# Kernel tuning notes

Hardware: AMD Instinct MI355X
Metric: run time of the kernel (lower is better)

The kernel has to match this reference:

```python
import jax, jax.numpy as jnp
import numpy as np

DIM = 384
HEADS = 12
WIN = (7, 7)
N = WIN[0] * WIN[1]
B = 4096
NW = 64  # number of windows sharing one mask


def _relative_position_index(win):
    wh, ww = win
    coords = np.stack(np.meshgrid(np.arange(wh), np.arange(ww), indexing='ij'))  # (2,wh,ww)
    flat = coords.reshape(2, -1)                                                 # (2, N)
    rel = flat[:, :, None] - flat[:, None, :]                                    # (2, N, N)
    rel = rel.transpose(1, 2, 0).astype(np.int64)
    rel[:, :, 0] += wh - 1
    rel[:, :, 1] += ww - 1
    rel[:, :, 0] *= 2 * ww - 1
    return jnp.asarray(rel.sum(-1), dtype=jnp.int32)                             # (N, N)


def setup_inputs() -> dict:
    key = jax.random.key(0)
    ks = jax.random.split(key, 7)
    std = 0.02
    return {
        'x': jax.random.normal(ks[0], (B, N, DIM), jnp.float32),
        'mask': jax.random.normal(ks[1], (NW, N, N), jnp.float32),
        'qkv_w': jax.random.normal(ks[2], (3 * DIM, DIM), jnp.float32) * std,
        'qkv_b': jnp.zeros((3 * DIM,), jnp.float32),
        'bias_table': jax.random.normal(ks[3], ((2 * WIN[0] - 1) * (2 * WIN[1] - 1), HEADS), jnp.float32) * std,
        'proj_w': jax.random.normal(ks[4], (DIM, DIM), jnp.float32) * std,
        'proj_b': jnp.zeros((DIM,), jnp.float32),
        'rel_idx': _relative_position_index(WIN),
    }


def reference(x, mask, qkv_w, qkv_b, bias_table, proj_w, proj_b, rel_idx):
    B_, n, c = x.shape
    h = HEADS
    d = c // h
    scale = d ** -0.5

    qkv = x @ qkv_w.T + qkv_b                                  # (B_, N, 3C)
    qkv = qkv.reshape(B_, n, 3, h, d).transpose(2, 0, 3, 1, 4)  # (3, B_, H, N, D)
    q, k, v = qkv[0], qkv[1], qkv[2]

    attn = jnp.einsum('bhnd,bhmd->bhnm', q, k) * scale          # (B_, H, N, N)

    bias = bias_table[rel_idx]                                  # (N, N, H)
    attn = attn + bias.transpose(2, 0, 1)[None]                 # add (1, H, N, N)

    nW = mask.shape[0]
    attn = attn.reshape(B_ // nW, nW, h, n, n) + mask[None, :, None]
    attn = attn.reshape(B_, h, n, n)

    attn = jax.nn.softmax(attn, axis=-1)
    out = jnp.einsum('bhnm,bhmd->bhnd', attn, v)                # (B_, H, N, D)
    out = out.transpose(0, 2, 1, 3).reshape(B_, n, c)
    return out @ proj_w.T + proj_b
```

## Files before the change

kernel.cpp:

```cpp
#include <hip/hip_runtime.h>

typedef __bf16 bf16;
typedef __bf16 bf16x4 __attribute__((ext_vector_type(4)));
typedef __bf16 bf16x8 __attribute__((ext_vector_type(8)));
typedef float f32x4 __attribute__((ext_vector_type(4)));
typedef float f32x16 __attribute__((ext_vector_type(16)));
typedef int i32x2 __attribute__((ext_vector_type(2)));
typedef unsigned int u32;

#define DIMC 384
#define NHEADS 12
#define NTOK 49
#define NWINB 4096
#define MROWS (NWINB*NTOK)

#define MFMA32(A,B,C) __builtin_amdgcn_mfma_f32_32x32x16_bf16(A,B,C,0,0,0)

#define GLOAD16(gsrc, lbase) \
  __builtin_amdgcn_global_load_lds( \
      (const __attribute__((address_space(1))) u32*)(gsrc), \
      (__attribute__((address_space(3))) u32*)(lbase), 16, 0, 0)

__global__ __launch_bounds__(256) void k_convert(const float4* __restrict__ in,
                                                 bf16x4* __restrict__ out, int n4) {
  int stride = gridDim.x * blockDim.x;
  for (int i = blockIdx.x * blockDim.x + threadIdx.x; i < n4; i += stride) {
    float4 v = in[i];
    bf16x4 o;
    o[0] = (bf16)v.x; o[1] = (bf16)v.y; o[2] = (bf16)v.z; o[3] = (bf16)v.w;
    out[i] = o;
  }
}

__global__ __launch_bounds__(256) void k_biasT(const float* __restrict__ table,
                                               const int* __restrict__ rel,
                                               float* __restrict__ outp) {
  int i = blockIdx.x * 256 + threadIdx.x;
  if (i < NHEADS * NTOK * NTOK) {
    int h = i / (NTOK * NTOK), r2 = i - h * (NTOK * NTOK);
    int key = r2 / NTOK, q = r2 - key * NTOK;
    outp[i] = table[rel[q * NTOK + key] * NHEADS + h];
  }
}

__global__ __launch_bounds__(256) void k_maskT(const float* __restrict__ mask,
                                               float* __restrict__ outp) {
  int i = blockIdx.x * 256 + threadIdx.x;
  if (i < 64 * NTOK * NTOK) {
    int w = i / (NTOK * NTOK), r2 = i - w * (NTOK * NTOK);
    int key = r2 / NTOK, q = r2 - key * NTOK;
    outp[i] = mask[(w * NTOK + q) * NTOK + key];
  }
}

template <int MODE>
__global__ __launch_bounds__(256) void k_gemm(const bf16* __restrict__ A,
                                              const bf16* __restrict__ Bw,
                                              const float* __restrict__ bias,
                                              bf16* __restrict__ oQ, bf16* __restrict__ oK,
                                              bf16* __restrict__ oV, float* __restrict__ oP) {
  __shared__ __align__(16) bf16 lA[2][64 * 64];
  __shared__ __align__(16) bf16 lB[2][128 * 64];
  const int t = threadIdx.x;
  const int l = t & 63;
  const int wv = t >> 6;
  const int wr = wv >> 1, wc = wv & 1;

  const u32 NXB = MODE == 0 ? 9 : 3;
  const u32 nwg = NXB * (MROWS / 64);
  u32 lin = blockIdx.y * gridDim.x + blockIdx.x;
  u32 logical = (lin & 7) * (nwg >> 3) + (lin >> 3);
  const int n0 = (int)(logical % NXB) * 128;
  const int m0 = (int)(logical / NXB) * 64;

  const int lr = l & 15, lg = l >> 4;

  const int srowA = wv * 16 + (l >> 3);
  const int srowB = wv * 32 + (l >> 3);
  const int scolb = (l & 7) * 16;

  f32x4 acc[2][4] = {};

#define STAGE(BUF, K0)                                                            \
  {                                                                               \
    _Pragma("unroll") for (int i = 0; i < 2; ++i) {                               \
      int row = srowA + i * 8;                                                    \
      int sc = (scolb ^ ((row & 7) << 4)) >> 1;                                   \
      GLOAD16(&A[(size_t)(m0 + row) * DIMC + (K0) + sc],                          \
              &lA[BUF][wv * 1024 + i * 512]);                                     \
    }                                                                             \
    _Pragma("unroll") for (int i = 0; i < 4; ++i) {                               \
      int row = srowB + i * 8;                                                    \
      int sc = (scolb ^ ((row & 7) << 4)) >> 1;                                   \
      GLOAD16(&Bw[(size_t)(n0 + row) * DIMC + (K0) + sc],                         \
              &lB[BUF][wv * 2048 + i * 512]);                                     \
    }                                                                             \
  }

  STAGE(0, 0);

#pragma unroll
  for (int tt = 0; tt < 6; ++tt) {
    const int cur = tt & 1;
    if (tt > 0) __builtin_amdgcn_s_barrier();
    if (tt < 5) {
      STAGE(cur ^ 1, (tt + 1) * 64);
      asm volatile("s_waitcnt vmcnt(6)" ::: "memory");
    } else {
      asm volatile("s_waitcnt vmcnt(0)" ::: "memory");
    }
    __builtin_amdgcn_s_barrier();

#pragma unroll
    for (int kk = 0; kk < 64; kk += 32) {
      bf16x8 af[2], bfv[4];
#pragma unroll
      for (int f = 0; f < 2; ++f) {
        int row = wr * 32 + f * 16 + lr;
        int cb = (kk + lg * 8) * 2;
        af[f] = *reinterpret_cast<const bf16x8*>(
            &lA[cur][row * 64 + ((cb ^ ((row & 7) << 4)) >> 1)]);
      }
#pragma unroll
      for (int f = 0; f < 4; ++f) {
        int row = wc * 64 + f * 16 + lr;
        int cb = (kk + lg * 8) * 2;
        bfv[f] = *reinterpret_cast<const bf16x8*>(
            &lB[cur][row * 64 + ((cb ^ ((row & 7) << 4)) >> 1)]);
      }
#pragma unroll
      for (int fm = 0; fm < 2; ++fm)
#pragma unroll
        for (int fn = 0; fn < 4; ++fn)
          acc[fm][fn] = __builtin_amdgcn_mfma_f32_16x16x32_bf16(af[fm], bfv[fn], acc[fm][fn], 0, 0, 0);
    }
  }
#undef STAGE

  const int cbase = n0 + wc * 64;
  const bf16* dummy;
  bf16* dst;
  int col0;
  if (MODE == 0) {
    int which = cbase / 384;
    dst = which == 0 ? oQ : (which == 1 ? oK : oV);
    col0 = cbase - which * 384;
  }
#pragma unroll
  for (int fn = 0; fn < 4; ++fn) {
    int c = cbase + fn * 16 + lr;
    float bc = bias[c];
#pragma unroll
    for (int fm = 0; fm < 2; ++fm) {
#pragma unroll
      for (int r = 0; r < 4; ++r) {
        int m = m0 + wr * 32 + fm * 16 + lg * 4 + r;
        float v = acc[fm][fn][r] + bc;
        if (MODE == 0) {
          dst[(size_t)m * 384 + col0 + fn * 16 + lr] = (bf16)v;
        } else {
          oP[(size_t)m * 384 + c] = v;
        }
      }
    }
  }
  (void)dummy;
}

__global__ __launch_bounds__(256, 4) void k_attn(const bf16* __restrict__ Q,
                                                 const bf16* __restrict__ K,
                                                 const bf16* __restrict__ V,
                                                 const float* __restrict__ biasT,
                                                 const float* __restrict__ maskT,
                                                 bf16* __restrict__ H) {
  __shared__ __align__(16) bf16 Vl[4][32 * 72];
  const int t = threadIdx.x, l = t & 63, wv = t >> 6;
  const int p = blockIdx.x * 4 + wv;
  const int b = p / 12, h = p - b * 12;
  const int w = b & 63;
  const size_t rbase = (size_t)b * 49 * 384 + h * 32;
  const int c = l & 31, b5 = l >> 5;
  bf16* vl = Vl[wv];

  {
    bf16x4 z = {};
    for (int i = l; i < 128; i += 64) {
      int d = i >> 2, kq = 48 + (i & 3) * 4;
      *reinterpret_cast<bf16x4*>(&vl[d * 72 + kq]) = z;
    }
  }
  for (int i = l; i < 392; i += 64) {
    int key = i >> 3, dc = (i & 7) * 4;
    bf16x4 vv = *reinterpret_cast<const bf16x4*>(&V[rbase + (size_t)key * 384 + dc]);
#pragma unroll
    for (int j = 0; j < 4; ++j) vl[(dc + j) * 72 + key] = vv[j];
  }

  bf16x8 kf[2][2], qf[2][2];
#pragma unroll
  for (int f = 0; f < 2; ++f) {
    int row = f * 32 + c; if (row > 48) row = 48;
#pragma unroll
    for (int kd = 0; kd < 2; ++kd) {
      kf[f][kd] = *reinterpret_cast<const bf16x8*>(&K[rbase + (size_t)row * 384 + kd * 16 + b5 * 8]);
      qf[f][kd] = *reinterpret_cast<const bf16x8*>(&Q[rbase + (size_t)row * 384 + kd * 16 + b5 * 8]);
    }
  }

  const float scale = 0.17677669529663689f;
  const float* bT = biasT + h * 2401;
  const float* mT = maskT + w * 2401;

#pragma unroll
  for (int fn = 0; fn < 2; ++fn) {
    f32x16 s0 = {}, s1 = {};
    s0 = MFMA32(kf[0][0], qf[fn][0], s0);
    s0 = MFMA32(kf[0][1], qf[fn][1], s0);
    s1 = MFMA32(kf[1][0], qf[fn][0], s1);
    s1 = MFMA32(kf[1][1], qf[fn][1], s1);

    int q = fn * 32 + c;
    int qc = q > 48 ? 48 : q;

    float vals[32];
    float vmax = -1e30f;
#pragma unroll
    for (int fm = 0; fm < 2; ++fm) {
#pragma unroll
      for (int r = 0; r < 16; ++r) {
        int key = fm * 32 + (r & 3) + 8 * (r >> 2) + 4 * b5;
        float sv = fm ? s1[r] : s0[r];
        float v;
        if (key < 49) {
          float cm = bT[key * 49 + qc] + mT[key * 49 + qc];
          v = fmaf(sv, scale, cm);
        } else {
          v = -1e30f;
        }
        vals[fm * 16 + r] = v;
        vmax = fmaxf(vmax, v);
      }
    }
    vmax = fmaxf(vmax, __shfl_xor(vmax, 32));
    float sum = 0.f;
#pragma unroll
    for (int i = 0; i < 32; ++i) {
      float e = __expf(vals[i] - vmax);
      vals[i] = e;
      sum += e;
    }
    sum += __shfl_xor(sum, 32);
    float inv = 1.f / sum;

    f32x16 o = {};
#pragma unroll
    for (int kk = 0; kk < 4; ++kk) {
      int ib = (kk >> 1) * 16 + 8 * (kk & 1);
      union { bf16 hh[2]; u32 u; } cv;
      u32 A0, A1, B0, B1;
      cv.hh[0] = (bf16)(vals[ib + 0] * inv); cv.hh[1] = (bf16)(vals[ib + 1] * inv); A0 = cv.u;
      cv.hh[0] = (bf16)(vals[ib + 2] * inv); cv.hh[1] = (bf16)(vals[ib + 3] * inv); A1 = cv.u;
      cv.hh[0] = (bf16)(vals[ib + 4] * inv); cv.hh[1] = (bf16)(vals[ib + 5] * inv); B0 = cv.u;
      cv.hh[0] = (bf16)(vals[ib + 6] * inv); cv.hh[1] = (bf16)(vals[ib + 7] * inv); B1 = cv.u;
      i32x2 sw0 = __builtin_amdgcn_permlane32_swap((int)A0, (int)B0, false, false);
      i32x2 sw1 = __builtin_amdgcn_permlane32_swap((int)A1, (int)B1, false, false);
      union { u32 d[4]; bf16x8 v8; } pa;
      pa.d[0] = (u32)sw0[0]; pa.d[1] = (u32)sw1[0];
      pa.d[2] = (u32)sw0[1]; pa.d[3] = (u32)sw1[1];
      bf16x8 vf = *reinterpret_cast<const bf16x8*>(&vl[c * 72 + kk * 16 + b5 * 8]);
      o = MFMA32(pa.v8, vf, o);
    }

#pragma unroll
    for (int r = 0; r < 16; ++r) {
      int qrow = fn * 32 + (r & 3) + 8 * (r >> 2) + 4 * b5;
      if (qrow < 49)
        H[((size_t)b * 49 + qrow) * 384 + h * 32 + c] = (bf16)o[r];
    }
  }
}

extern "C" void kernel_launch(void* const* d_in, const int* in_sizes, int n_in,
                              void* d_out, int out_size, void* d_ws, size_t ws_size,
                              hipStream_t stream) {
  const float* x     = (const float*)d_in[0];
  const float* mask  = (const float*)d_in[1];
  const float* qkvw  = (const float*)d_in[2];
  const float* qkvb  = (const float*)d_in[3];
  const float* btab  = (const float*)d_in[4];
  const float* projw = (const float*)d_in[5];
  const float* projb = (const float*)d_in[6];
  const int*   rel   = (const int*)d_in[7];
  float* out = (float*)d_out;

  const size_t NELEM = (size_t)MROWS * DIMC;
  char* ws = (char*)d_ws;
  bf16*  xb    = (bf16*)ws;
  bf16*  vb    = (bf16*)(ws + 154140672);
  float* biasT = (float*)(ws + 308281344);
  bf16*  wqkv  = (bf16*)(ws + 308396800);
  float* maskT = (float*)(ws + 308396800);
  bf16*  wproj = (bf16*)(ws + 309281536);
  bf16* qb = (bf16*)d_out;
  bf16* kb = qb + NELEM;

  k_convert<<<2048, 256, 0, stream>>>((const float4*)x, (bf16x4*)xb, (int)(NELEM / 4));
  k_convert<<<432, 256, 0, stream>>>((const float4*)qkvw, (bf16x4*)wqkv, 3 * DIMC * DIMC / 4);
  k_convert<<<144, 256, 0, stream>>>((const float4*)projw, (bf16x4*)wproj, DIMC * DIMC / 4);
  k_biasT<<<(NHEADS * NTOK * NTOK + 255) / 256, 256, 0, stream>>>(btab, rel, biasT);

  k_gemm<0><<<dim3(9, MROWS / 64), 256, 0, stream>>>(xb, wqkv, qkvb, qb, kb, vb, nullptr);
  k_maskT<<<(64 * NTOK * NTOK + 255) / 256, 256, 0, stream>>>(mask, maskT);
  k_attn<<<(NWINB * NHEADS) / 4, 256, 0, stream>>>(qb, kb, vb, biasT, maskT, xb);
  k_gemm<1><<<dim3(3, MROWS / 64), 256, 0, stream>>>(xb, wproj, projb, nullptr, nullptr, nullptr, out);
}
```

Before: 889.9 us.

## Fuse window attention with output projection in one per-window kernel

Adds k_attn_proj, where each block handles one window: it computes all 12 heads' attention into a swizzled 64x384 bf16 LDS tile and then runs the output projection from LDS, writing the final fp32 output directly. This drops the global write and re-read of the attention output and the separate projection GEMM launch. Q and K now go to workspace instead of the output buffer, so the fused path only runs when the workspace is large enough, with the old path kept as a fallback. The cost is about 53KB of LDS per block, which lowers occupancy, and projection weights read straight from global or L2 with no LDS staging.

Measured after the change: 969.4 us. 1.09x slower.

```diff
diff --git a/kernel.cpp b/kernel.cpp
--- a/kernel.cpp
+++ b/kernel.cpp
@@ -138,9 +138,8 @@
 #undef STAGE
 
   const int cbase = n0 + wc * 64;
-  const bf16* dummy;
-  bf16* dst;
-  int col0;
+  bf16* dst = nullptr;
+  int col0 = 0;
   if (MODE == 0) {
     int which = cbase / 384;
     dst = which == 0 ? oQ : (which == 1 ? oK : oV);
@@ -164,7 +163,6 @@
       }
     }
   }
-  (void)dummy;
 }
 
 __global__ __launch_bounds__(256, 4) void k_attn(const bf16* __restrict__ Q,
@@ -280,6 +278,156 @@
   }
 }
 
+__global__ __launch_bounds__(256) void k_attn_proj(
+    const bf16* __restrict__ Q, const bf16* __restrict__ K,
+    const bf16* __restrict__ V, const float* __restrict__ biasT,
+    const float* __restrict__ maskT, const bf16* __restrict__ Wp,
+    const float* __restrict__ projb, float* __restrict__ OUT) {
+  __shared__ __align__(16) bf16 Vl[4][32 * 72];
+  __shared__ __align__(16) bf16 hl[64 * 384];
+  const int t = threadIdx.x, l = t & 63, wv = t >> 6;
+  const int b = blockIdx.x;
+  const int w = b & 63;
+  const int c = l & 31, b5 = l >> 5;
+  bf16* vl = Vl[wv];
+  const float scale = 0.17677669529663689f;
+  const float* mT = maskT + w * 2401;
+
+  {
+    bf16x4 z = {};
+    for (int i = l; i < 128; i += 64) {
+      int d = i >> 2, kq = 48 + (i & 3) * 4;
+      *reinterpret_cast<bf16x4*>(&vl[d * 72 + kq]) = z;
+    }
+  }
+
+  for (int hi = 0; hi < 3; ++hi) {
+    const int h = hi * 4 + wv;
+    const size_t rbase = (size_t)b * 49 * 384 + h * 32;
+    const float* bT = biasT + h * 2401;
+
+    for (int i = l; i < 392; i += 64) {
+      int key = i >> 3, dc = (i & 7) * 4;
+      bf16x4 vv = *reinterpret_cast<const bf16x4*>(&V[rbase + (size_t)key * 384 + dc]);
+#pragma unroll
+      for (int j = 0; j < 4; ++j) vl[(dc + j) * 72 + key] = vv[j];
+    }
+
+    bf16x8 kf[2][2], qf[2][2];
+#pragma unroll
+    for (int f = 0; f < 2; ++f) {
+      int row = f * 32 + c; if (row > 48) row = 48;
+#pragma unroll
+      for (int kd = 0; kd < 2; ++kd) {
+        kf[f][kd] = *reinterpret_cast<const bf16x8*>(&K[rbase + (size_t)row * 384 + kd * 16 + b5 * 8]);
+        qf[f][kd] = *reinterpret_cast<const bf16x8*>(&Q[rbase + (size_t)row * 384 + kd * 16 + b5 * 8]);
+      }
+    }
+
+#pragma unroll
+    for (int fn = 0; fn < 2; ++fn) {
+      f32x16 s0 = {}, s1 = {};
+      s0 = MFMA32(kf[0][0], qf[fn][0], s0);
+      s0 = MFMA32(kf[0][1], qf[fn][1], s0);
+      s1 = MFMA32(kf[1][0], qf[fn][0], s1);
+      s1 = MFMA32(kf[1][1], qf[fn][1], s1);
+
+      int q = fn * 32 + c;
+      int qc = q > 48 ? 48 : q;
+
+      float vals[32];
+      float vmax = -1e30f;
+#pragma unroll
+      for (int fm = 0; fm < 2; ++fm) {
+#pragma unroll
+        for (int r = 0; r < 16; ++r) {
+          int key = fm * 32 + (r & 3) + 8 * (r >> 2) + 4 * b5;
+          float sv = fm ? s1[r] : s0[r];
+          float v;
+          if (key < 49) {
+            float cm = bT[key * 49 + qc] + mT[key * 49 + qc];
+            v = fmaf(sv, scale, cm);
+          } else {
+            v = -1e30f;
+          }
+          vals[fm * 16 + r] = v;
+          vmax = fmaxf(vmax, v);
+        }
+      }
+      vmax = fmaxf(vmax, __shfl_xor(vmax, 32));
+      float sum = 0.f;
+#pragma unroll
+      for (int i = 0; i < 32; ++i) {
+        float e = __expf(vals[i] - vmax);
+        vals[i] = e;
+        sum += e;
+      }
+      sum += __shfl_xor(sum, 32);
+      float inv = 1.f / sum;
+
+      f32x16 o = {};
+#pragma unroll
+      for (int kk = 0; kk < 4; ++kk) {
+        int ib = (kk >> 1) * 16 + 8 * (kk & 1);
+        union { bf16 hh[2]; u32 u; } cv;
+        u32 A0, A1, B0, B1;
+        cv.hh[0] = (bf16)(vals[ib + 0] * inv); cv.hh[1] = (bf16)(vals[ib + 1] * inv); A0 = cv.u;
+        cv.hh[0] = (bf16)(vals[ib + 2] * inv); cv.hh[1] = (bf16)(vals[ib + 3] * inv); A1 = cv.u;
+        cv.hh[0] = (bf16)(vals[ib + 4] * inv); cv.hh[1] = (bf16)(vals[ib + 5] * inv); B0 = cv.u;
+        cv.hh[0] = (bf16)(vals[ib + 6] * inv); cv.hh[1] = (bf16)(vals[ib + 7] * inv); B1 = cv.u;
+        i32x2 sw0 = __builtin_amdgcn_permlane32_swap((int)A0, (int)B0, false, false);
+        i32x2 sw1 = __builtin_amdgcn_permlane32_swap((int)A1, (int)B1, false, false);
+        union { u32 d[4]; bf16x8 v8; } pa;
+        pa.d[0] = (u32)sw0[0]; pa.d[1] = (u32)sw1[0];
+        pa.d[2] = (u32)sw0[1]; pa.d[3] = (u32)sw1[1];
+        bf16x8 vf = *reinterpret_cast<const bf16x8*>(&vl[c * 72 + kk * 16 + b5 * 8]);
+        o = MFMA32(pa.v8, vf, o);
+      }
+
+#pragma unroll
+      for (int r = 0; r < 16; ++r) {
+        int qrow = fn * 32 + (r & 3) + 8 * (r >> 2) + 4 * b5;
+        int cb = (h * 64 + 2 * c) ^ ((qrow & 15) << 4);
+        *reinterpret_cast<bf16*>(reinterpret_cast<char*>(hl) + qrow * 768 + cb) = (bf16)o[r];
+      }
+    }
+  }
+  __syncthreads();
+
+  f32x16 pacc[2][3] = {};
+  const int col0 = wv * 96;
+#pragma unroll
+  for (int fn = 0; fn < 3; ++fn) {
+    const int col = col0 + fn * 32 + c;
+#pragma unroll
+    for (int ks = 0; ks < 24; ++ks) {
+      bf16x8 wf = *reinterpret_cast<const bf16x8*>(&Wp[(size_t)col * 384 + ks * 16 + b5 * 8]);
+#pragma unroll
+      for (int fm = 0; fm < 2; ++fm) {
+        int row = fm * 32 + c;
+        int cb = (ks * 32 + b5 * 16) ^ ((row & 15) << 4);
+        bf16x8 hf = *reinterpret_cast<const bf16x8*>(
+            reinterpret_cast<const char*>(hl) + row * 768 + cb);
+        pacc[fm][fn] = MFMA32(hf, wf, pacc[fm][fn]);
+      }
+    }
+  }
+#pragma unroll
+  for (int fn = 0; fn < 3; ++fn) {
+    int col = col0 + fn * 32 + c;
+    float bc = projb[col];
+#pragma unroll
+    for (int fm = 0; fm < 2; ++fm) {
+#pragma unroll
+      for (int r = 0; r < 16; ++r) {
+        int m = fm * 32 + (r & 3) + 8 * (r >> 2) + 4 * b5;
+        if (m < 49)
+          OUT[((size_t)b * 49 + m) * 384 + col] = pacc[fm][fn][r] + bc;
+      }
+    }
+  }
+}
+
 extern "C" void kernel_launch(void* const* d_in, const int* in_sizes, int n_in,
                               void* d_out, int out_size, void* d_ws, size_t ws_size,
                               hipStream_t stream) {
@@ -293,24 +441,46 @@
   const int*   rel   = (const int*)d_in[7];
   float* out = (float*)d_out;
 
-  const size_t NELEM = (size_t)MROWS * DIMC;
+  const size_t NB = 154140672;
   char* ws = (char*)d_ws;
-  bf16*  xb    = (bf16*)ws;
-  bf16*  vb    = (bf16*)(ws + 154140672);
-  float* biasT = (float*)(ws + 308281344);
-  bf16*  wqkv  = (bf16*)(ws + 308396800);
-  float* maskT = (float*)(ws + 308396800);
-  bf16*  wproj = (bf16*)(ws + 309281536);
-  bf16* qb = (bf16*)d_out;
-  bf16* kb = qb + NELEM;
-
-  k_convert<<<2048, 256, 0, stream>>>((const float4*)x, (bf16x4*)xb, (int)(NELEM / 4));
-  k_convert<<<432, 256, 0, stream>>>((const float4*)qkvw, (bf16x4*)wqkv, 3 * DIMC * DIMC / 4);
-  k_convert<<<144, 256, 0, stream>>>((const float4*)projw, (bf16x4*)wproj, DIMC * DIMC / 4);
-  k_biasT<<<(NHEADS * NTOK * NTOK + 255) / 256, 256, 0, stream>>>(btab, rel, biasT);
-
-  k_gemm<0><<<dim3(9, MROWS / 64), 256, 0, stream>>>(xb, wqkv, qkvb, qb, kb, vb, nullptr);
-  k_maskT<<<(64 * NTOK * NTOK + 255) / 256, 256, 0, stream>>>(mask, maskT);
-  k_attn<<<(NWINB * NHEADS) / 4, 256, 0, stream>>>(qb, kb, vb, biasT, maskT, xb);
-  k_gemm<1><<<dim3(3, MROWS / 64), 256, 0, stream>>>(xb, wproj, projb, nullptr, nullptr, nullptr, out);
-}
+  const size_t FUSED_WS = 4 * NB + 115456 + 884736 + 294912;
+
+  if (ws_size >= FUSED_WS) {
+    bf16*  xb    = (bf16*)ws;
+    bf16*  qb    = (bf16*)(ws + NB);
+    bf16*  kb    = (bf16*)(ws + 2 * NB);
+    bf16*  vb    = (bf16*)(ws + 3 * NB);
+    float* biasT = (float*)(ws + 4 * NB);
+    bf16*  wqkv  = (bf16*)(ws + 4 * NB + 115456);
+    float* maskT = (float*)(ws + 4 * NB + 115456);
+    bf16*  wproj = (bf16*)(ws + 4 * NB + 115456 + 884736);
+
+    k_convert<<<2048, 256, 0, stream>>>((const float4*)x, (bf16x4*)xb, (int)(NB / 2 / 4));
+    k_convert<<<432, 256, 0, stream>>>((const float4*)qkvw, (bf16x4*)wqkv, 3 * DIMC * DIMC / 4);
+    k_convert<<<144, 256, 0, stream>>>((const float4*)projw, (bf16x4*)wproj, DIMC * DIMC / 4);
+    k_biasT<<<(NHEADS * NTOK * NTOK + 255) / 256, 256, 0, stream>>>(btab, rel, biasT);
+
+    k_gemm<0><<<dim3(9, MROWS / 64), 256, 0, stream>>>(xb, wqkv, qkvb, qb, kb, vb, nullptr);
+    k_maskT<<<(64 * NTOK * NTOK + 255) / 256, 256, 0, stream>>>(mask, maskT);
+    k_attn_proj<<<NWINB, 256, 0, stream>>>(qb, kb, vb, biasT, maskT, wproj, projb, out);
+  } else {
+    bf16*  xb    = (bf16*)ws;
+    bf16*  vb    = (bf16*)(ws + NB);
+    float* biasT = (float*)(ws + 2 * NB);
+    bf16*  wqkv  = (bf16*)(ws + 2 * NB + 115456);
+    float* maskT = (float*)(ws + 2 * NB + 115456);
+    bf16*  wproj = (bf16*)(ws + 2 * NB + 115456 + 884736);
+    bf16* qb = (bf16*)d_out;
+    bf16* kb = qb + NB / 2;
+
+    k_convert<<<2048, 256, 0, stream>>>((const float4*)x, (bf16x4*)xb, (int)(NB / 2 / 4));
+    k_convert<<<432, 256, 0, stream>>>((const float4*)qkvw, (bf16x4*)wqkv, 3 * DIMC * DIMC / 4);
+    k_convert<<<144, 256, 0, stream>>>((const float4*)projw, (bf16x4*)wproj, DIMC * DIMC / 4);
+    k_biasT<<<(NHEADS * NTOK * NTOK + 255) / 256, 256, 0, stream>>>(btab, rel, biasT);
+
+    k_gemm<0><<<dim3(9, MROWS / 64), 256, 0, stream>>>(xb, wqkv, qkvb, qb, kb, vb, nullptr);
+    k_maskT<<<(64 * NTOK * NTOK + 255) / 256, 256, 0, stream>>>(mask, maskT);
+    k_attn<<<(NWINB * NHEADS) / 4, 256, 0, stream>>>(qb, kb, vb, biasT, maskT, xb);
+    k_gemm<1><<<dim3(3, MROWS / 64), 256, 0, stream>>>(xb, wproj, projb, nullptr, nullptr, nullptr, out);
+  }
+}
```

## Emit head-major Q/K and pre-transposed padded V from QKV GEMM epilogue

Applied to the files above, without the earlier changes.

The QKV GEMM epilogue now scatters Q and K into per-(window,head) contiguous blocks and writes V already transposed into a zero-padded 32x64 per-head tile. The attention kernel can then load V fragments straight into registers, dropping the LDS staging and transpose. Bias and mask are also pre-summed into one per-(head,window) table, so each score needs one gather instead of two. In exchange the GEMM stores become scattered, narrow 2-byte writes (the V ones especially). A full zeroing pass over a larger V buffer and a bigger combined bias/mask table add memory traffic.

New measurement: 947.2 us. 1.06x slower.

```diff
diff --git a/kernel.cpp b/kernel.cpp
--- a/kernel.cpp
+++ b/kernel.cpp
@@ -32,24 +32,22 @@
   }
 }
 
-__global__ __launch_bounds__(256) void k_biasT(const float* __restrict__ table,
-                                               const int* __restrict__ rel,
-                                               float* __restrict__ outp) {
+__global__ __launch_bounds__(256) void k_zero(float4* __restrict__ p, int n4) {
+  int stride = gridDim.x * blockDim.x;
+  float4 z = {0.f, 0.f, 0.f, 0.f};
+  for (int i = blockIdx.x * blockDim.x + threadIdx.x; i < n4; i += stride) p[i] = z;
+}
+
+__global__ __launch_bounds__(256) void k_bm(const float* __restrict__ table,
+                                            const int* __restrict__ rel,
+                                            const float* __restrict__ mask,
+                                            float* __restrict__ outp) {
   int i = blockIdx.x * 256 + threadIdx.x;
-  if (i < NHEADS * NTOK * NTOK) {
-    int h = i / (NTOK * NTOK), r2 = i - h * (NTOK * NTOK);
+  if (i < NHEADS * 64 * NTOK * NTOK) {
+    int hw = i / 2401, r2 = i - hw * 2401;
+    int h = hw >> 6, w = hw & 63;
     int key = r2 / NTOK, q = r2 - key * NTOK;
-    outp[i] = table[rel[q * NTOK + key] * NHEADS + h];
-  }
-}
-
-__global__ __launch_bounds__(256) void k_maskT(const float* __restrict__ mask,
-                                               float* __restrict__ outp) {
-  int i = blockIdx.x * 256 + threadIdx.x;
-  if (i < 64 * NTOK * NTOK) {
-    int w = i / (NTOK * NTOK), r2 = i - w * (NTOK * NTOK);
-    int key = r2 / NTOK, q = r2 - key * NTOK;
-    outp[i] = mask[(w * NTOK + q) * NTOK + key];
+    outp[i] = table[rel[q * NTOK + key] * NHEADS + h] + mask[(w * NTOK + q) * NTOK + key];
   }
 }
 
@@ -138,63 +136,64 @@
 #undef STAGE
 
   const int cbase = n0 + wc * 64;
-  const bf16* dummy;
-  bf16* dst;
-  int col0;
   if (MODE == 0) {
-    int which = cbase / 384;
-    dst = which == 0 ? oQ : (which == 1 ? oK : oV);
-    col0 = cbase - which * 384;
-  }
-#pragma unroll
-  for (int fn = 0; fn < 4; ++fn) {
-    int c = cbase + fn * 16 + lr;
-    float bc = bias[c];
-#pragma unroll
-    for (int fm = 0; fm < 2; ++fm) {
-#pragma unroll
-      for (int r = 0; r < 4; ++r) {
-        int m = m0 + wr * 32 + fm * 16 + lg * 4 + r;
-        float v = acc[fm][fn][r] + bc;
-        if (MODE == 0) {
-          dst[(size_t)m * 384 + col0 + fn * 16 + lr] = (bf16)v;
-        } else {
-          oP[(size_t)m * 384 + c] = v;
+    const int which = cbase / 384;
+    const int colh = cbase - which * 384;
+#pragma unroll
+    for (int fn = 0; fn < 4; ++fn) {
+      const int cc = colh + fn * 16 + lr;
+      const int h = cc >> 5, d = cc & 31;
+      const float bc = bias[cbase + fn * 16 + lr];
+#pragma unroll
+      for (int fm = 0; fm < 2; ++fm) {
+#pragma unroll
+        for (int r = 0; r < 4; ++r) {
+          const int m = m0 + wr * 32 + fm * 16 + lg * 4 + r;
+          const int bi = m / 49, n = m - bi * 49;
+          const size_t p = (size_t)bi * 12 + h;
+          const float v = acc[fm][fn][r] + bc;
+          if (which < 2) {
+            bf16* dst = which == 0 ? oQ : oK;
+            dst[(p * 49 + n) * 32 + d] = (bf16)v;
+          } else {
+            oV[p * 2048 + d * 64 + n] = (bf16)v;
+          }
         }
       }
     }
-  }
-  (void)dummy;
+  } else {
+#pragma unroll
+    for (int fn = 0; fn < 4; ++fn) {
+      const int c = cbase + fn * 16 + lr;
+      const float bc = bias[c];
+#pragma unroll
+      for (int fm = 0; fm < 2; ++fm) {
+#pragma unroll
+        for (int r = 0; r < 4; ++r) {
+          const int m = m0 + wr * 32 + fm * 16 + lg * 4 + r;
+          oP[(size_t)m * 384 + c] = acc[fm][fn][r] + bc;
+        }
+      }
+    }
+  }
 }
 
 __global__ __launch_bounds__(256, 4) void k_attn(const bf16* __restrict__ Q,
                                                  const bf16* __restrict__ K,
-                                                 const bf16* __restrict__ V,
-                                                 const float* __restrict__ biasT,
-                                                 const float* __restrict__ maskT,
+                                                 const bf16* __restrict__ VT,
+                                                 const float* __restrict__ bmT,
                                                  bf16* __restrict__ H) {
-  __shared__ __align__(16) bf16 Vl[4][32 * 72];
   const int t = threadIdx.x, l = t & 63, wv = t >> 6;
   const int p = blockIdx.x * 4 + wv;
   const int b = p / 12, h = p - b * 12;
   const int w = b & 63;
-  const size_t rbase = (size_t)b * 49 * 384 + h * 32;
+  const size_t base = (size_t)p * (49 * 32);
   const int c = l & 31, b5 = l >> 5;
-  bf16* vl = Vl[wv];
-
-  {
-    bf16x4 z = {};
-    for (int i = l; i < 128; i += 64) {
-      int d = i >> 2, kq = 48 + (i & 3) * 4;
-      *reinterpret_cast<bf16x4*>(&vl[d * 72 + kq]) = z;
-    }
-  }
-  for (int i = l; i < 392; i += 64) {
-    int key = i >> 3, dc = (i & 7) * 4;
-    bf16x4 vv = *reinterpret_cast<const bf16x4*>(&V[rbase + (size_t)key * 384 + dc]);
-#pragma unroll
-    for (int j = 0; j < 4; ++j) vl[(dc + j) * 72 + key] = vv[j];
-  }
+
+  bf16x8 vf[4];
+#pragma unroll
+  for (int kk = 0; kk < 4; ++kk)
+    vf[kk] = *reinterpret_cast<const bf16x8*>(&VT[(size_t)p * 2048 + c * 64 + kk * 16 + b5 * 8]);
 
   bf16x8 kf[2][2], qf[2][2];
 #pragma unroll
@@ -202,14 +201,13 @@
     int row = f * 32 + c; if (row > 48) row = 48;
 #pragma unroll
     for (int kd = 0; kd < 2; ++kd) {
-      kf[f][kd] = *reinterpret_cast<const bf16x8*>(&K[rbase + (size_t)row * 384 + kd * 16 + b5 * 8]);
-      qf[f][kd] = *reinterpret_cast<const bf16x8*>(&Q[rbase + (size_t)row * 384 + kd * 16 + b5 * 8]);
+      kf[f][kd] = *reinterpret_cast<const bf16x8*>(&K[base + row * 32 + kd * 16 + b5 * 8]);
+      qf[f][kd] = *reinterpret_cast<const bf16x8*>(&Q[base + row * 32 + kd * 16 + b5 * 8]);
     }
   }
 
   const float scale = 0.17677669529663689f;
-  const float* bT = biasT + h * 2401;
-  const float* mT = maskT + w * 2401;
+  const float* bm = bmT + ((size_t)h * 64 + w) * 2401;
 
 #pragma unroll
   for (int fn = 0; fn < 2; ++fn) {
@@ -232,8 +230,7 @@
         float sv = fm ? s1[r] : s0[r];
         float v;
         if (key < 49) {
-          float cm = bT[key * 49 + qc] + mT[key * 49 + qc];
-          v = fmaf(sv, scale, cm);
+          v = fmaf(sv, scale, bm[key * 49 + qc]);
         } else {
           v = -1e30f;
         }
@@ -267,8 +264,7 @@
       union { u32 d[4]; bf16x8 v8; } pa;
       pa.d[0] = (u32)sw0[0]; pa.d[1] = (u32)sw1[0];
       pa.d[2] = (u32)sw0[1]; pa.d[3] = (u32)sw1[1];
-      bf16x8 vf = *reinterpret_cast<const bf16x8*>(&vl[c * 72 + kk * 16 + b5 * 8]);
-      o = MFMA32(pa.v8, vf, o);
+      o = MFMA32(pa.v8, vf[kk], o);
     }
 
 #pragma unroll
@@ -293,24 +289,25 @@
   const int*   rel   = (const int*)d_in[7];
   float* out = (float*)d_out;
 
-  const size_t NELEM = (size_t)MROWS * DIMC;
+  const size_t NB  = 154140672;
+  const size_t VTB = 201326592;
+  const size_t BMB = 7375872;
   char* ws = (char*)d_ws;
   bf16*  xb    = (bf16*)ws;
-  bf16*  vb    = (bf16*)(ws + 154140672);
-  float* biasT = (float*)(ws + 308281344);
-  bf16*  wqkv  = (bf16*)(ws + 308396800);
-  float* maskT = (float*)(ws + 308396800);
-  bf16*  wproj = (bf16*)(ws + 309281536);
+  bf16*  vT    = (bf16*)(ws + NB);
+  float* bmT   = (float*)(ws + NB + VTB);
+  bf16*  wqkv  = (bf16*)(ws + NB + VTB + BMB);
+  bf16*  wproj = (bf16*)(ws + NB + VTB + BMB + 884736);
   bf16* qb = (bf16*)d_out;
-  bf16* kb = qb + NELEM;
-
-  k_convert<<<2048, 256, 0, stream>>>((const float4*)x, (bf16x4*)xb, (int)(NELEM / 4));
+  bf16* kb = qb + NB / 2;
+
+  k_convert<<<2048, 256, 0, stream>>>((const float4*)x, (bf16x4*)xb, (int)(NB / 8));
   k_convert<<<432, 256, 0, stream>>>((const float4*)qkvw, (bf16x4*)wqkv, 3 * DIMC * DIMC / 4);
   k_convert<<<144, 256, 0, stream>>>((const float4*)projw, (bf16x4*)wproj, DIMC * DIMC / 4);
-  k_biasT<<<(NHEADS * NTOK * NTOK + 255) / 256, 256, 0, stream>>>(btab, rel, biasT);
-
-  k_gemm<0><<<dim3(9, MROWS / 64), 256, 0, stream>>>(xb, wqkv, qkvb, qb, kb, vb, nullptr);
-  k_maskT<<<(64 * NTOK * NTOK + 255) / 256, 256, 0, stream>>>(mask, maskT);
-  k_attn<<<(NWINB * NHEADS) / 4, 256, 0, stream>>>(qb, kb, vb, biasT, maskT, xb);
+  k_bm<<<(NHEADS * 64 * NTOK * NTOK + 255) / 256, 256, 0, stream>>>(btab, rel, mask, bmT);
+  k_zero<<<2048, 256, 0, stream>>>((float4*)vT, (int)(VTB / 16));
+
+  k_gemm<0><<<dim3(9, MROWS / 64), 256, 0, stream>>>(xb, wqkv, qkvb, qb, kb, vT, nullptr);
+  k_attn<<<(NWINB * NHEADS) / 4, 256, 0, stream>>>(qb, kb, vT, bmT, xb);
   k_gemm<1><<<dim3(3, MROWS / 64), 256, 0, stream>>>(xb, wproj, projb, nullptr, nullptr, nullptr, out);
 }
```
